# Optimization experiments

Measured on AMD Instinct MI355X. Metric: run time of the kernel, lower is better.

## Reference

```python
import jax, jax.numpy as jnp
import numpy as np

L, H, N, F, E, FF, OUT, B = 4, 8, 1024, 128, 128, 512, 64, 32


def setup_inputs() -> dict:
    key = jax.random.key(0)
    ks = jax.random.split(key, 16)
    s = 0.02
    return {
        "x": jax.random.normal(ks[0], (B, N, F), jnp.float32),
        "adj": jax.random.randint(ks[1], (N, N), 0, 2, jnp.int32),
        "Ws": jax.random.normal(ks[2], (L, H, E, F), jnp.float32) * s,
        "bs": jnp.zeros((L, H, E), jnp.float32),
        "As": jax.random.normal(ks[3], (L, H, 2 * E, N), jnp.float32) * s,
        "W1": jax.random.normal(ks[4], (L, FF, F), jnp.float32) * s,
        "b1": jnp.zeros((L, FF), jnp.float32),
        "W2": jax.random.normal(ks[5], (L, F, FF), jnp.float32) * s,
        "b2": jnp.zeros((L, F), jnp.float32),
        "g1": jnp.ones((L, F), jnp.float32),
        "be1": jnp.zeros((L, F), jnp.float32),
        "g2": jnp.ones((L, F), jnp.float32),
        "be2": jnp.zeros((L, F), jnp.float32),
        "Wo": jax.random.normal(ks[6], (OUT, N * F), jnp.float32) * s,
        "bo": jnp.zeros((OUT,), jnp.float32),
    }


def _ln(x, g, b, eps=1e-5):
    m = jnp.mean(x, axis=-1, keepdims=True)
    v = jnp.mean((x - m) ** 2, axis=-1, keepdims=True)
    return (x - m) / jnp.sqrt(v + eps) * g + b


def reference(x, adj, Ws, bs, As, W1, b1, W2, b2, g1, be1, g2, be2, Wo, bo):
    # mask[j, i] = 1 if j is a neighbor of i (adj_matrix[:, i] > 0 in torch source)
    mask = (adj > 0).astype(x.dtype)
    E_ = Ws.shape[2]
    for l in range(Ws.shape[0]):
        # per-head projection: h [B, H, N, E]
        h = jnp.einsum('bnf,hef->bhne', x, Ws[l]) + bs[l][None, :, None, :]
        # score[b,h,i] = h_i . a[:E, i] + (sum_{j in N(i)} h_j) . a[E:, i]
        s1 = jnp.einsum('bhne,hen->bhn', h, As[l][:, :E_, :])
        hn = jnp.einsum('jn,bhje->bhne', mask, h)  # neighbor sums
        s2 = jnp.einsum('bhne,hen->bhn', hn, As[l][:, E_:, :])
        score = s1 + s2  # [B, H, N]
        # attention row i is the constant score[b,h,i] broadcast over columns,
        # so attention @ h == score[...,None] * h.sum(over nodes)
        hsum = h.sum(axis=2)  # [B, H, E]
        hp = score[..., None] * hsum[:, :, None, :]  # [B, H, N, E]
        att = jax.nn.leaky_relu(hp, 0.01).sum(axis=1)  # sum over heads -> [B, N, F]
        x = _ln(x + att, g1[l], be1[l])
        ff = jax.nn.relu(x @ W1[l].T + b1[l]) @ W2[l].T + b2[l]
        x = _ln(x + ff, g2[l], be2[l])
    flat = x.reshape(x.shape[0], -1)  # [B, N*F]
    return jax.nn.relu(flat) @ Wo.T + bo
```

## Files before the change

### kernel.cpp

```cpp
#include <hip/hip_runtime.h>

#define L_ 4
#define H_ 8
#define Nn 1024
#define F_ 128
#define E_ 128
#define FF_ 512
#define OUT_ 64
#define B_ 32
#define KTOT (Nn * F_)

typedef unsigned short u16;
typedef __bf16 bf16_t;
typedef __attribute__((ext_vector_type(8))) __bf16 bf16x8;
typedef __attribute__((ext_vector_type(4))) float f32x4;

__device__ __forceinline__ u16 f2b(float v) {
    bf16_t h = (bf16_t)v;
    return __builtin_bit_cast(u16, h);
}

typedef const __attribute__((address_space(1))) void* gvp;
typedef __attribute__((address_space(3))) void* lvp;
__device__ __forceinline__ void gll16(const void* g, void* l) {
    __builtin_amdgcn_global_load_lds((gvp)g, (lvp)l, 16, 0, 0);
}

template <int R>
__device__ __forceinline__ void stage(const u16* __restrict__ g, int ldg,
                                      u16* lds, int w, int l) {
    const int r8 = l >> 3, jq = l & 7;
#pragma unroll
    for (int i = 0; i < R / 32; ++i) {
        const int row0 = w * (R / 4) + i * 8;
        const int row = row0 + r8;
        gll16(g + (long)row * ldg + ((jq ^ (row & 7)) << 3), lds + row0 * 64);
    }
}

template <int BM, int BN, bool DUAL, int EPI, int BSH, bool GSWAP, bool DBUF>
__global__ __launch_bounds__(256) void k_mfma(
    const u16* __restrict__ A, int lda, long sAz,
    const u16* __restrict__ Bhp, const u16* __restrict__ Blp, int ldb, long sBz,
    const float* __restrict__ bias,
    float* __restrict__ Cf, u16* __restrict__ Cb, int ldc, long sCz, int K)
{
    constexpr int WN = (BN == 64) ? 1 : ((BM == 64) ? 4 : 2);
    constexpr int WM = 4 / WN;
    constexpr int SM = BM / WM, SN = BN / WN;
    constexpr int MF = SM / 16, NF = SN / 16;
    constexpr int BUFE = BM * 64 + (DUAL ? 2 : 1) * BN * 64;
    __shared__ __align__(16) u16 lds[BUFE * (DBUF ? 2 : 1)];
    const int t = threadIdx.x;
    const int w = t >> 6, l = t & 63, lr = l & 15, lg = l >> 4;
    const int wm0 = (w / WN) * SM, wn0 = (w % WN) * SN;
    const int bidm = GSWAP ? blockIdx.z : blockIdx.x;
    const int bidz = GSWAP ? blockIdx.x : blockIdx.z;
    const int m0 = bidm * BM, n0 = blockIdx.y * BN;
    A += BSH ? ((long)(bidz >> 1) * sAz + (long)(bidz & 1) * 128)
             : (long)bidz * sAz;
    Bhp += (long)(bidz >> BSH) * sBz;
    if (DUAL) Blp += (long)bidz * sBz;

    f32x4 acc[MF][NF] = {};

    auto stageAll = [&](u16* base, int k0) {
        stage<BM>(A + (long)m0 * lda + k0, lda, base, w, l);
        stage<BN>(Bhp + (long)n0 * ldb + k0, ldb, base + BM * 64, w, l);
        if (DUAL) stage<BN>(Blp + (long)n0 * ldb + k0, ldb, base + BM * 64 + BN * 64, w, l);
    };
    auto compute = [&](const u16* base) {
        const u16* Al = base;
        const u16* Bh = base + BM * 64;
        const u16* Bl = Bh + BN * 64;
#pragma unroll
        for (int ks = 0; ks < 2; ++ks) {
            bf16x8 af[MF], bh[NF], bl[NF];
            const int kq = ks * 4 + lg;
#pragma unroll
            for (int mf = 0; mf < MF; ++mf) {
                int row = wm0 + mf * 16 + lr;
                af[mf] = *reinterpret_cast<const bf16x8*>(&Al[row * 64 + ((kq ^ (row & 7)) << 3)]);
            }
#pragma unroll
            for (int nf = 0; nf < NF; ++nf) {
                int row = wn0 + nf * 16 + lr;
                int off = row * 64 + ((kq ^ (row & 7)) << 3);
                bh[nf] = *reinterpret_cast<const bf16x8*>(&Bh[off]);
                if (DUAL) bl[nf] = *reinterpret_cast<const bf16x8*>(&Bl[off]);
            }
#pragma unroll
            for (int mf = 0; mf < MF; ++mf)
#pragma unroll
                for (int nf = 0; nf < NF; ++nf) {
                    acc[mf][nf] = __builtin_amdgcn_mfma_f32_16x16x32_bf16(af[mf], bh[nf], acc[mf][nf], 0, 0, 0);
                    if (DUAL)
                        acc[mf][nf] = __builtin_amdgcn_mfma_f32_16x16x32_bf16(af[mf], bl[nf], acc[mf][nf], 0, 0, 0);
                }
        }
    };

    if (DBUF) {
        stageAll(lds, 0);
        __syncthreads();
        int cur = 0;
        for (int k0 = 0; k0 < K; k0 += 64) {
            if (k0 + 64 < K) stageAll(lds + (cur ^ 1) * BUFE, k0 + 64);
            compute(lds + cur * BUFE);
            __syncthreads();
            cur ^= 1;
        }
    } else {
        for (int k0 = 0; k0 < K; k0 += 64) {
            __syncthreads();
            stageAll(lds, k0);
            __syncthreads();
            compute(lds);
        }
    }

    float bv[NF];
    if (EPI) {
#pragma unroll
        for (int nf = 0; nf < NF; ++nf) bv[nf] = bias[n0 + wn0 + nf * 16 + lr];
    }
    if (EPI == 1) Cb += (long)bidz * sCz;
    else          Cf += (long)bidz * sCz;
#pragma unroll
    for (int mf = 0; mf < MF; ++mf)
#pragma unroll
        for (int nf = 0; nf < NF; ++nf)
#pragma unroll
            for (int r = 0; r < 4; ++r) {
                long row = m0 + wm0 + mf * 16 + lg * 4 + r;
                int col = n0 + wn0 + nf * 16 + lr;
                float v = acc[mf][nf][r];
                if (EPI) v += bv[nf];
                if (EPI == 1) Cb[row * ldc + col] = f2b(fmaxf(v, 0.f));
                else          Cf[row * ldc + col] = v;
            }
}

template <bool LAST>
__global__ __launch_bounds__(256) void k_ff_ln2(
    const u16* __restrict__ xb,
    const u16* __restrict__ W1b,
    const float* __restrict__ b1,
    const u16* __restrict__ W2b,
    const float* __restrict__ b2,
    float* __restrict__ xc,
    const float* __restrict__ g, const float* __restrict__ be,
    u16* __restrict__ xh, u16* __restrict__ xl,
    float* __restrict__ xsp,
    u16* __restrict__ xrb)
{
    __shared__ __align__(16) u16 lds[18432];
    const int t = threadIdx.x;
    const int w = t >> 6, l = t & 63, lr = l & 15, lg = l >> 4;
    const int wn0 = w * 32;
    const int m0 = blockIdx.x * 64;
    u16* A0 = lds;
    u16* P0 = lds + 8192;

    stage<64>(xb + (long)m0 * F_,      F_, A0, w, l);
    stage<64>(xb + (long)m0 * F_ + 64, F_, A0 + 4096, w, l);
    __syncthreads();

    f32x4 acc2[4][2] = {};
    for (int c = 0; c < 4; ++c) {
        f32x4 acc1[4][2] = {};
#pragma unroll
        for (int s = 0; s < 4; ++s) {
            const int kh = s >> 1, kq = (s & 1) * 4 + lg;
            bf16x8 af[4], bfr[2];
#pragma unroll
            for (int mf = 0; mf < 4; ++mf) {
                int row = mf * 16 + lr;
                af[mf] = *reinterpret_cast<const bf16x8*>(
                    &A0[kh * 4096 + row * 64 + ((kq ^ (row & 7)) << 3)]);
            }
#pragma unroll
            for (int nf = 0; nf < 2; ++nf) {
                int row = c * 128 + wn0 + nf * 16 + lr;
                bfr[nf] = *reinterpret_cast<const bf16x8*>(
                    &W1b[(long)row * F_ + s * 32 + lg * 8]);
            }
#pragma unroll
            for (int mf = 0; mf < 4; ++mf)
#pragma unroll
                for (int nf = 0; nf < 2; ++nf)
                    acc1[mf][nf] = __builtin_amdgcn_mfma_f32_16x16x32_bf16(af[mf], bfr[nf], acc1[mf][nf], 0, 0, 0);
        }
        __syncthreads();
        float b1v[2] = { b1[c * 128 + wn0 + lr], b1[c * 128 + wn0 + 16 + lr] };
#pragma unroll
        for (int mf = 0; mf < 4; ++mf)
#pragma unroll
            for (int nf = 0; nf < 2; ++nf)
#pragma unroll
                for (int r = 0; r < 4; ++r) {
                    int row = mf * 16 + lg * 4 + r;
                    int cc = wn0 + nf * 16 + lr;
                    int c6 = cc & 63;
                    float v = fmaxf(acc1[mf][nf][r] + b1v[nf], 0.f);
                    P0[(cc >> 6) * 4096 + row * 64 + ((((c6 >> 3) ^ (row & 7))) << 3) + (c6 & 7)] = f2b(v);
                }
        __syncthreads();
#pragma unroll
        for (int s = 0; s < 4; ++s) {
            const int kh = s >> 1, kq = (s & 1) * 4 + lg;
            bf16x8 af[4], bfr[2];
#pragma unroll
            for (int mf = 0; mf < 4; ++mf) {
                int row = mf * 16 + lr;
                af[mf] = *reinterpret_cast<const bf16x8*>(
                    &P0[kh * 4096 + row * 64 + ((kq ^ (row & 7)) << 3)]);
            }
#pragma unroll
            for (int nf = 0; nf < 2; ++nf) {
                int row = wn0 + nf * 16 + lr;
                bfr[nf] = *reinterpret_cast<const bf16x8*>(
                    &W2b[(long)row * FF_ + c * 128 + s * 32 + lg * 8]);
            }
#pragma unroll
            for (int mf = 0; mf < 4; ++mf)
#pragma unroll
                for (int nf = 0; nf < 2; ++nf)
                    acc2[mf][nf] = __builtin_amdgcn_mfma_f32_16x16x32_bf16(af[mf], bfr[nf], acc2[mf][nf], 0, 0, 0);
        }
    }
    __syncthreads();
    float (*buf)[132] = (float(*)[132])lds;
    float (*ps)[128]  = (float(*)[128])((char*)lds + 34816);
    float bv[2] = { b2[wn0 + lr], b2[wn0 + 16 + lr] };
#pragma unroll
    for (int mf = 0; mf < 4; ++mf)
#pragma unroll
        for (int nf = 0; nf < 2; ++nf)
#pragma unroll
            for (int r = 0; r < 4; ++r)
                buf[mf * 16 + lg * 4 + r][wn0 + nf * 16 + lr] = acc2[mf][nf][r] + bv[nf];
    __syncthreads();
    const float gl0 = g[l], gl1 = g[l + 64], bl0 = be[l], bl1 = be[l + 64];
    float s0 = 0.f, s1 = 0.f;
#pragma unroll
    for (int rr = 0; rr < 16; ++rr) {
        const int row = w * 16 + rr;
        const long xb_ = (long)(m0 + row) * F_;
        float v0 = buf[row][l] + xc[xb_ + l];
        float v1 = buf[row][l + 64] + xc[xb_ + l + 64];
        float sum = v0 + v1;
#pragma unroll
        for (int o = 32; o; o >>= 1) sum += __shfl_xor(sum, o);
        const float mean = sum * (1.f / 128.f);
        const float d0 = v0 - mean, d1 = v1 - mean;
        float vs = d0 * d0 + d1 * d1;
#pragma unroll
        for (int o = 32; o; o >>= 1) vs += __shfl_xor(vs, o);
        const float rstd = rsqrtf(vs * (1.f / 128.f) + 1e-5f);
        float o0 = d0 * rstd * gl0 + bl0;
        float o1 = d1 * rstd * gl1 + bl1;
        if (LAST) {
            xrb[xb_ + l] = f2b(fmaxf(o0, 0.f));
            xrb[xb_ + l + 64] = f2b(fmaxf(o1, 0.f));
        } else {
            xc[xb_ + l] = o0;       xc[xb_ + l + 64] = o1;
            buf[row][l] = o0;       buf[row][l + 64] = o1;
            s0 += o0;               s1 += o1;
        }
    }
    if (!LAST) {
        ps[w][l] = s0; ps[w][l + 64] = s1;
        __syncthreads();
        const int b = m0 >> 10, nb0 = m0 & 1023, seg = (m0 >> 6) & 15;
        const int n8 = (t & 7) * 8, fb = t >> 3;
#pragma unroll
        for (int i = 0; i < 4; ++i) {
            const int f = fb + 32 * i;
            union { u16 u[8]; float4 v; } Hv, Lv;
#pragma unroll
            for (int j = 0; j < 8; ++j) {
                float v = buf[n8 + j][f];
                bf16_t h = (bf16_t)v;
                Hv.u[j] = __builtin_bit_cast(u16, h);
                Lv.u[j] = f2b(v - (float)h);
            }
            const long ob = ((long)b * F_ + f) * Nn + nb0 + n8;
            *reinterpret_cast<float4*>(&xh[ob]) = Hv.v;
            *reinterpret_cast<float4*>(&xl[ob]) = Lv.v;
        }
        if (t < 128)
            xsp[((long)b * 16 + seg) * 128 + t] =
                ps[0][t] + ps[1][t] + ps[2][t] + ps[3][t];
    }
}

__global__ __launch_bounds__(256) void k_final_mfma(
    const u16* __restrict__ xrb, const u16* __restrict__ Wob,
    float* __restrict__ part)
{
    __shared__ __align__(16) u16 Al[32 * 512];
    const int c = blockIdx.x;
    const long k0 = (long)c * 512;
    const int t = threadIdx.x, w = t >> 6, l = t & 63, lr = l & 15, lg = l >> 4;
#pragma unroll
    for (int i = 0; i < 8; ++i) {
        int ch = i * 256 + t, row = ch >> 6, jq = ch & 63;
        *reinterpret_cast<float4*>(&Al[row * 512 + ((jq ^ (row & 7)) << 3)]) =
            *reinterpret_cast<const float4*>(&xrb[(long)row * KTOT + k0 + (jq << 3)]);
    }
    __syncthreads();
    f32x4 acc[2] = {};
    const u16* Bp = Wob + (long)(w * 16 + lr) * KTOT + k0 + lg * 8;
#pragma unroll
    for (int ks = 0; ks < 16; ++ks) {
        bf16x8 bfr = *reinterpret_cast<const bf16x8*>(Bp + ks * 32);
        const int j8 = ks * 4 + lg;
#pragma unroll
        for (int mf = 0; mf < 2; ++mf) {
            int row = mf * 16 + lr;
            bf16x8 af = *reinterpret_cast<const bf16x8*>(&Al[row * 512 + ((j8 ^ (row & 7)) << 3)]);
            acc[mf] = __builtin_amdgcn_mfma_f32_16x16x32_bf16(af, bfr, acc[mf], 0, 0, 0);
        }
    }
#pragma unroll
    for (int mf = 0; mf < 2; ++mf)
#pragma unroll
        for (int r = 0; r < 4; ++r) {
            int b = mf * 16 + lg * 4 + r, o = w * 16 + lr;
            part[((long)c * B_ + b) * OUT_ + o] = acc[mf][r];
        }
}

__global__ void k_final_reduce(const float* __restrict__ part,
                               const float* __restrict__ bo, float* __restrict__ out)
{
    int i = blockIdx.x * 256 + threadIdx.x;
    int o = i & 63;
    float s = bo[o];
    for (int c = 0; c < 256; ++c) s += part[(long)c * (B_ * OUT_) + i];
    out[i] = s;
}

__global__ __launch_bounds__(256) void k_maskT(const int* __restrict__ adj,
                                               u16* __restrict__ maskTb,
                                               int* __restrict__ degi)
{
    __shared__ u16 tl[64][65];
    const int j0 = blockIdx.x * 64, n0 = blockIdx.y * 64, t = threadIdx.x;
#pragma unroll
    for (int i = 0; i < 16; ++i) {
        int s = i * 256 + t, jl = s >> 6, nl = s & 63;
        tl[jl][nl] = (adj[(long)(j0 + jl) * Nn + n0 + nl] > 0) ? 0x3F80 : 0;
    }
    __syncthreads();
    if (t < 64) {
        int c = 0;
#pragma unroll
        for (int jl = 0; jl < 64; ++jl) c += (tl[jl][t] != 0);
        atomicAdd(&degi[n0 + t], c);
    }
#pragma unroll
    for (int i = 0; i < 16; ++i) {
        int s = i * 256 + t, nl = s >> 6, jl = s & 63;
        maskTb[(long)(n0 + nl) * Nn + j0 + jl] = tl[jl][nl];
    }
}

__global__ __launch_bounds__(256) void k_tpb(const float* __restrict__ in,
                                             u16* __restrict__ out, int R, int C)
{
    __shared__ float tl[64][65];
    const int c0 = blockIdx.x * 64, r0 = blockIdx.y * 64, t = threadIdx.x;
    in  += (long)blockIdx.z * R * C;
    out += (long)blockIdx.z * R * C;
#pragma unroll
    for (int i = 0; i < 16; ++i) {
        int s = i * 256 + t, rl = s >> 6, cl = s & 63;
        tl[rl][cl] = in[(long)(r0 + rl) * C + c0 + cl];
    }
    __syncthreads();
#pragma unroll
    for (int i = 0; i < 16; ++i) {
        int s = i * 256 + t, cl = s >> 6, rl = s & 63;
        out[(long)(c0 + cl) * R + r0 + rl] = f2b(tl[rl][cl]);
    }
}

__global__ void k_cvtW(const float* __restrict__ W1, const float* __restrict__ W2,
                       u16* __restrict__ W1b, u16* __restrict__ W2b)
{
    int i = blockIdx.x * 256 + threadIdx.x;
    W1b[i] = f2b(W1[i]);
    W2b[i] = f2b(W2[i]);
}

__global__ void k_cvtWo(const float* __restrict__ Wo, u16* __restrict__ Wob)
{
    long i = ((long)blockIdx.x * 256 + threadIdx.x) * 8;
    float4 a = *reinterpret_cast<const float4*>(&Wo[i]);
    float4 b = *reinterpret_cast<const float4*>(&Wo[i + 4]);
    union { u16 u[8]; float4 v; } r;
    r.u[0] = f2b(a.x); r.u[1] = f2b(a.y); r.u[2] = f2b(a.z); r.u[3] = f2b(a.w);
    r.u[4] = f2b(b.x); r.u[5] = f2b(b.y); r.u[6] = f2b(b.z); r.u[7] = f2b(b.w);
    *reinterpret_cast<float4*>(&Wob[i]) = r.v;
}

__global__ __launch_bounds__(256) void k_xpose(const float* __restrict__ x,
                                               u16* __restrict__ xh, u16* __restrict__ xl)
{
    __shared__ float tile[64][132];
    const int b = blockIdx.y, n0 = blockIdx.x * 64, t = threadIdx.x;
#pragma unroll
    for (int i = 0; i < 8; ++i) {
        int s = i * 256 + t, nl = s >> 5, f4 = (s & 31) << 2;
        float4 v = *reinterpret_cast<const float4*>(&x[((long)b * Nn + n0 + nl) * F_ + f4]);
        tile[nl][f4] = v.x; tile[nl][f4 + 1] = v.y;
        tile[nl][f4 + 2] = v.z; tile[nl][f4 + 3] = v.w;
    }
    __syncthreads();
    const int f = t >> 1, nb = (t & 1) << 5;
    const long ob = ((long)b * F_ + f) * Nn + n0 + nb;
    union { u16 u[8]; float4 v; } Hv, Lv;
#pragma unroll
    for (int i = 0; i < 32; i += 8) {
#pragma unroll
        for (int j = 0; j < 8; ++j) {
            float v = tile[nb + i + j][f];
            bf16_t h = (bf16_t)v;
            Hv.u[j] = __builtin_bit_cast(u16, h);
            Lv.u[j] = f2b(v - (float)h);
        }
        *reinterpret_cast<float4*>(&xh[ob + i]) = Hv.v;
        *reinterpret_cast<float4*>(&xl[ob + i]) = Lv.v;
    }
}

__global__ __launch_bounds__(256) void k_xs2(const float* __restrict__ x, float* __restrict__ xsp)
{
    __shared__ float sh[2][128];
    const int seg = blockIdx.x, b = blockIdx.y, t = threadIdx.x;
    const int f = t & 127, h2 = t >> 7;
    const float* p = x + ((long)b * Nn + seg * 64 + h2 * 32) * F_ + f;
    float s = 0.f;
    for (int i = 0; i < 32; ++i) s += p[(long)i * F_];
    sh[h2][f] = s;
    __syncthreads();
    if (t < 128) xsp[((long)b * 16 + seg) * 128 + t] = sh[0][t] + sh[1][t];
}

__global__ void k_hsum(const float* __restrict__ xsp, const float* __restrict__ Wl,
                       const float* __restrict__ bsl, float* __restrict__ hsum)
{
    __shared__ float xs[128];
    const int i = blockIdx.x * 256 + threadIdx.x;
    const int b = i >> 10;
    if (threadIdx.x < 128) {
        const float* xp = xsp + (long)b * 16 * 128 + threadIdx.x;
        float v = 0.f;
#pragma unroll
        for (int sg = 0; sg < 16; ++sg) v += xp[sg * 128];
        xs[threadIdx.x] = v;
    }
    __syncthreads();
    const int e = i & 127, h = (i >> 7) & 7;
    const float* w = Wl + ((long)h * E_ + e) * F_;
    float s = 0.f;
    for (int f = 0; f < F_; ++f) s += xs[f] * w[f];
    hsum[i] = s + (float)Nn * bsl[h * E_ + e];
}

__global__ void k_d12(const float* __restrict__ As, const float* __restrict__ bs,
                      float* __restrict__ d12all)
{
    const int lyr = blockIdx.y;
    const float* Asl = As + (long)lyr * H_ * 2 * E_ * Nn;
    const float* bsl = bs + (long)lyr * H_ * E_;
    int i = blockIdx.x * 256 + threadIdx.x;
    int n = i & 1023, h = (i >> 10) & 7, w = i >> 13;
    const float* a = Asl + ((long)h * 2 * E_ + (long)w * E_) * Nn + n;
    const float* bb = bsl + h * E_;
    float s = 0.f;
    for (int e = 0; e < E_; ++e) s += bb[e] * a[(long)e * Nn];
    d12all[(long)lyr * 2 * H_ * Nn + ((long)w * H_ + h) * Nn + n] = s;
}

__global__ __launch_bounds__(256) void k_score_ln1(
    float* __restrict__ x, const float* __restrict__ y,
    const float* __restrict__ Ct, const float* __restrict__ d12,
    const int* __restrict__ degi, const float* __restrict__ hsum,
    const float* __restrict__ g, const float* __restrict__ be,
    u16* __restrict__ xb)
{
    const int n = blockIdx.x, t = threadIdx.x;
    __shared__ float c1[H_][128], c2[H_][128];
    __shared__ float sbs[H_];
#pragma unroll
    for (int i = 0; i < 4; ++i) {
        int s = i * 256 + t, h = s >> 7, f = s & 127;
        c1[h][f] = Ct[((long)(2 * h) * Nn + n) * F_ + f];
        c2[h][f] = Ct[((long)(2 * h + 1) * Nn + n) * F_ + f];
    }
    if (t < H_) sbs[t] = d12[(long)t * Nn + n] + (float)degi[n] * d12[(long)(H_ + t) * Nn + n];
    __syncthreads();
    const int w = t >> 6, l = t & 63;
    const float gl0 = g[l], gl1 = g[l + 64], bl0 = be[l], bl1 = be[l + 64];
    for (int bi = 0; bi < 8; ++bi) {
        const int b = w * 8 + bi;
        const long base = ((long)b * Nn + n) * F_;
        float x0 = x[base + l], x1 = x[base + l + 64];
        float y0 = y[base + l], y1 = y[base + l + 64];
        float a0 = 0.f, a1 = 0.f;
#pragma unroll
        for (int h = 0; h < H_; ++h) {
            float p = x0 * c1[h][l] + x1 * c1[h][l + 64]
                    + y0 * c2[h][l] + y1 * c2[h][l + 64];
#pragma unroll
            for (int o = 32; o; o >>= 1) p += __shfl_xor(p, o);
            float s = p + sbs[h];
            float h0 = hsum[((long)b * H_ + h) * E_ + l];
            float h1 = hsum[((long)b * H_ + h) * E_ + l + 64];
            float p0 = s * h0, p1 = s * h1;
            a0 += (p0 > 0.f ? p0 : 0.01f * p0);
            a1 += (p1 > 0.f ? p1 : 0.01f * p1);
        }
        float v0 = x0 + a0, v1 = x1 + a1;
        float sum = v0 + v1;
#pragma unroll
        for (int o = 32; o; o >>= 1) sum += __shfl_xor(sum, o);
        const float mean = sum * (1.f / 128.f);
        const float d0 = v0 - mean, d1 = v1 - mean;
        float vs = d0 * d0 + d1 * d1;
#pragma unroll
        for (int o = 32; o; o >>= 1) vs += __shfl_xor(vs, o);
        const float rstd = rsqrtf(vs * (1.f / 128.f) + 1e-5f);
        float o0 = d0 * rstd * gl0 + bl0;
        float o1 = d1 * rstd * gl1 + bl1;
        x[base + l] = o0;        x[base + l + 64] = o1;
        xb[base + l] = f2b(o0);  xb[base + l + 64] = f2b(o1);
    }
}

extern "C" void kernel_launch(void* const* d_in, const int* in_sizes, int n_in,
                              void* d_out, int out_size, void* d_ws, size_t ws_size,
                              hipStream_t stream)
{
    const float* x_in = (const float*)d_in[0];
    const int*   adj  = (const int*)d_in[1];
    const float* Ws   = (const float*)d_in[2];
    const float* bs   = (const float*)d_in[3];
    const float* As   = (const float*)d_in[4];
    const float* W1   = (const float*)d_in[5];
    const float* b1   = (const float*)d_in[6];
    const float* W2   = (const float*)d_in[7];
    const float* b2   = (const float*)d_in[8];
    const float* g1   = (const float*)d_in[9];
    const float* be1  = (const float*)d_in[10];
    const float* g2   = (const float*)d_in[11];
    const float* be2  = (const float*)d_in[12];
    const float* Wo   = (const float*)d_in[13];
    const float* bo   = (const float*)d_in[14];
    float* out = (float*)d_out;

    char* wsb = (char*)d_ws;
    u16*   maskTb = (u16*)wsb;
    float* xc     = (float*)(wsb + (2L << 20));
    float* y      = (float*)(wsb + (18L << 20));
    float* CtAll  = (float*)(wsb + (66L << 20));
    u16*   xb     = (u16*)(wsb + (98L << 20));
    u16*   xrb    = (u16*)(wsb + (106L << 20));
    u16*   Wob    = (u16*)(wsb + (114L << 20));
    float* part   = (float*)(wsb + (130L << 20));
    u16*   xTh    = (u16*)(wsb + (132L << 20));
    u16*   xTl    = (u16*)(wsb + (140L << 20));
    u16*   AsTb   = (u16*)(wsb + (148L << 20));
    u16*   WsTb   = (u16*)(wsb + (164L << 20));
    char*  S      = wsb + (166L << 20);
    int*   degi   = (int*)S;
    float* xsp    = (float*)(S + (4L << 10));
    float* hsum   = (float*)(S + (260L << 10));
    float* d12all = (float*)(S + (388L << 10));
    u16*   W1b    = (u16*)(S + (644L << 10));
    u16*   W2b    = (u16*)(S + (1156L << 10));

    hipMemsetAsync(degi, 0, Nn * sizeof(int), stream);
    hipMemcpyAsync(xc, x_in, sizeof(float) * (long)B_ * Nn * F_,
                   hipMemcpyDeviceToDevice, stream);
    k_maskT<<<dim3(16, 16), 256, 0, stream>>>(adj, maskTb, degi);
    k_cvtW<<<(L_ * FF_ * F_) / 256, 256, 0, stream>>>(W1, W2, W1b, W2b);
    k_cvtWo<<<(OUT_ * KTOT) / (256 * 8), 256, 0, stream>>>(Wo, Wob);
    k_tpb<<<dim3(16, 4, L_ * H_), 256, 0, stream>>>(As, AsTb, 2 * E_, Nn);
    k_tpb<<<dim3(2, 2, L_ * H_), 256, 0, stream>>>(Ws, WsTb, E_, F_);
    k_xpose<<<dim3(16, B_), 256, 0, stream>>>(x_in, xTh, xTl);
    k_xs2<<<dim3(16, B_), 256, 0, stream>>>(x_in, xsp);
    k_d12<<<dim3((2 * H_ * Nn) / 256, L_), 256, 0, stream>>>(As, bs, d12all);
    k_mfma<64, 128, false, 0, 1, false, false><<<dim3(16, 1, 64), 256, 0, stream>>>(
        AsTb, 2 * E_, (long)Nn * 2 * E_, WsTb, nullptr, E_, (long)F_ * E_,
        nullptr, CtAll, nullptr, F_, (long)Nn * F_, E_);

    for (int l = 0; l < L_; ++l) {
        const float* Wl  = Ws + (long)l * H_ * E_ * F_;
        const float* bsl = bs + (long)l * H_ * E_;

        k_mfma<128, 64, true, 0, 0, true, true><<<dim3(32, 2, 8), 256, 0, stream>>>(
            maskTb, Nn, 0L, xTh, xTl, Nn, (long)F_ * Nn,
            nullptr, y, nullptr, F_, (long)Nn * F_, Nn);

        k_hsum<<<(B_ * H_ * E_) / 256, 256, 0, stream>>>(xsp, Wl, bsl, hsum);
        k_score_ln1<<<Nn, 256, 0, stream>>>(
            xc, y, CtAll + (long)l * 16 * Nn * F_, d12all + (long)l * 2 * H_ * Nn,
            degi, hsum, g1 + l * F_, be1 + l * F_, xb);
        if (l < L_ - 1)
            k_ff_ln2<false><<<512, 256, 0, stream>>>(
                xb, W1b + (long)l * FF_ * F_, b1 + l * FF_,
                W2b + (long)l * F_ * FF_, b2 + l * F_, xc,
                g2 + l * F_, be2 + l * F_, xTh, xTl, xsp, nullptr);
        else
            k_ff_ln2<true><<<512, 256, 0, stream>>>(
                xb, W1b + (long)l * FF_ * F_, b1 + l * FF_,
                W2b + (long)l * F_ * FF_, b2 + l * F_, xc,
                g2 + l * F_, be2 + l * F_, nullptr, nullptr, nullptr, xrb);
    }

    k_final_mfma<<<256, 256, 0, stream>>>(xrb, Wob, part);
    k_final_reduce<<<(B_ * OUT_) / 256, 256, 0, stream>>>(part, bo, out);
}
```

Baseline: 412.2 us.

## Give each wave its own 16 rows in fused FFN+LN kernel, dropping block barriers

Restructures the fused FFN/LayerNorm kernel so each wave owns 16 rows and computes all 128 output columns, with weights as the MFMA A operand and activations as B (a transposed product). The hidden activation goes through a private per-wave LDS slice, which removes the block-wide __syncthreads between GEMM phases. LayerNorm now runs directly on the accumulator registers with vectorized residual and parameter loads, instead of going through an LDS staging buffer. In exchange, each wave reads four times as many weight fragments from global/L2, and the column-sum reduction becomes a 64-row serial loop over LDS.

```diff
diff --git a/kernel.cpp b/kernel.cpp
--- a/kernel.cpp
+++ b/kernel.cpp
@@ -154,123 +154,114 @@
     float* __restrict__ xsp,
     u16* __restrict__ xrb)
 {
-    __shared__ __align__(16) u16 lds[18432];
+    __shared__ __align__(16) u16 lds[16896];
     const int t = threadIdx.x;
     const int w = t >> 6, l = t & 63, lr = l & 15, lg = l >> 4;
-    const int wn0 = w * 32;
     const int m0 = blockIdx.x * 64;
-    u16* A0 = lds;
-    u16* P0 = lds + 8192;
-
-    stage<64>(xb + (long)m0 * F_,      F_, A0, w, l);
-    stage<64>(xb + (long)m0 * F_ + 64, F_, A0 + 4096, w, l);
-    __syncthreads();
-
-    f32x4 acc2[4][2] = {};
+    const int M0 = m0 + w * 16;
+    u16* xw = lds + w * 2048;
+    u16* pw = lds + 8192 + w * 2176;
+
+    {
+        const int r8 = l >> 3, jq = l & 7;
+#pragma unroll
+        for (int h = 0; h < 2; ++h)
+#pragma unroll
+            for (int i = 0; i < 2; ++i) {
+                const int row = i * 8 + r8;
+                gll16(xb + (long)(M0 + row) * F_ + h * 64 + ((jq ^ (row & 7)) << 3),
+                      xw + h * 1024 + i * 512);
+            }
+    }
+    asm volatile("s_waitcnt vmcnt(0)" ::: "memory");
+
+    f32x4 acc2[8] = {};
     for (int c = 0; c < 4; ++c) {
-        f32x4 acc1[4][2] = {};
+        f32x4 acc1[8] = {};
 #pragma unroll
         for (int s = 0; s < 4; ++s) {
             const int kh = s >> 1, kq = (s & 1) * 4 + lg;
-            bf16x8 af[4], bfr[2];
-#pragma unroll
-            for (int mf = 0; mf < 4; ++mf) {
-                int row = mf * 16 + lr;
-                af[mf] = *reinterpret_cast<const bf16x8*>(
-                    &A0[kh * 4096 + row * 64 + ((kq ^ (row & 7)) << 3)]);
+            bf16x8 xf = *reinterpret_cast<const bf16x8*>(
+                &xw[kh * 1024 + lr * 64 + ((kq ^ (lr & 7)) << 3)]);
+#pragma unroll
+            for (int nf = 0; nf < 8; ++nf) {
+                bf16x8 wf = *reinterpret_cast<const bf16x8*>(
+                    &W1b[(long)(c * 128 + nf * 16 + lr) * F_ + s * 32 + lg * 8]);
+                acc1[nf] = __builtin_amdgcn_mfma_f32_16x16x32_bf16(wf, xf, acc1[nf], 0, 0, 0);
             }
-#pragma unroll
-            for (int nf = 0; nf < 2; ++nf) {
-                int row = c * 128 + wn0 + nf * 16 + lr;
-                bfr[nf] = *reinterpret_cast<const bf16x8*>(
-                    &W1b[(long)row * F_ + s * 32 + lg * 8]);
+        }
+#pragma unroll
+        for (int nf = 0; nf < 8; ++nf) {
+            f32x4 bb = *reinterpret_cast<const f32x4*>(&b1[c * 128 + nf * 16 + lg * 4]);
+            union { u16 u[4]; uint2 q; } pk;
+#pragma unroll
+            for (int r = 0; r < 4; ++r)
+                pk.u[r] = f2b(fmaxf(acc1[nf][r] + bb[r], 0.f));
+            *reinterpret_cast<uint2*>(&pw[lr * 136 + nf * 16 + lg * 4]) = pk.q;
+        }
+#pragma unroll
+        for (int s2 = 0; s2 < 4; ++s2) {
+            bf16x8 pf = *reinterpret_cast<const bf16x8*>(&pw[lr * 136 + s2 * 32 + lg * 8]);
+#pragma unroll
+            for (int nf = 0; nf < 8; ++nf) {
+                bf16x8 wf = *reinterpret_cast<const bf16x8*>(
+                    &W2b[(long)(nf * 16 + lr) * FF_ + c * 128 + s2 * 32 + lg * 8]);
+                acc2[nf] = __builtin_amdgcn_mfma_f32_16x16x32_bf16(wf, pf, acc2[nf], 0, 0, 0);
             }
-#pragma unroll
-            for (int mf = 0; mf < 4; ++mf)
-#pragma unroll
-                for (int nf = 0; nf < 2; ++nf)
-                    acc1[mf][nf] = __builtin_amdgcn_mfma_f32_16x16x32_bf16(af[mf], bfr[nf], acc1[mf][nf], 0, 0, 0);
-        }
+        }
+    }
+
+    const long Mrow = (long)M0 + lr;
+    f32x4 vv[8];
+    float sum = 0.f;
+#pragma unroll
+    for (int nf = 0; nf < 8; ++nf) {
+        f32x4 rsd = *reinterpret_cast<const f32x4*>(&xc[Mrow * F_ + nf * 16 + lg * 4]);
+        f32x4 bb  = *reinterpret_cast<const f32x4*>(&b2[nf * 16 + lg * 4]);
+#pragma unroll
+        for (int r = 0; r < 4; ++r) {
+            vv[nf][r] = acc2[nf][r] + bb[r] + rsd[r];
+            sum += vv[nf][r];
+        }
+    }
+    sum += __shfl_xor(sum, 16);
+    sum += __shfl_xor(sum, 32);
+    const float mean = sum * (1.f / 128.f);
+    float vs = 0.f;
+#pragma unroll
+    for (int nf = 0; nf < 8; ++nf)
+#pragma unroll
+        for (int r = 0; r < 4; ++r) {
+            float d = vv[nf][r] - mean;
+            vs += d * d;
+        }
+    vs += __shfl_xor(vs, 16);
+    vs += __shfl_xor(vs, 32);
+    const float rstd = rsqrtf(vs * (1.f / 128.f) + 1e-5f);
+#pragma unroll
+    for (int nf = 0; nf < 8; ++nf) {
+        f32x4 gg = *reinterpret_cast<const f32x4*>(&g[nf * 16 + lg * 4]);
+        f32x4 bz = *reinterpret_cast<const f32x4*>(&be[nf * 16 + lg * 4]);
+        f32x4 o;
+#pragma unroll
+        for (int r = 0; r < 4; ++r)
+            o[r] = (vv[nf][r] - mean) * rstd * gg[r] + bz[r];
+        if (LAST) {
+            union { u16 u[4]; uint2 q; } pk;
+#pragma unroll
+            for (int r = 0; r < 4; ++r) pk.u[r] = f2b(fmaxf(o[r], 0.f));
+            *reinterpret_cast<uint2*>(&xrb[Mrow * F_ + nf * 16 + lg * 4]) = pk.q;
+        } else {
+            *reinterpret_cast<f32x4*>(&xc[Mrow * F_ + nf * 16 + lg * 4]) = o;
+            vv[nf] = o;
+        }
+    }
+    if (!LAST) {
         __syncthreads();
-        float b1v[2] = { b1[c * 128 + wn0 + lr], b1[c * 128 + wn0 + 16 + lr] };
-#pragma unroll
-        for (int mf = 0; mf < 4; ++mf)
-#pragma unroll
-            for (int nf = 0; nf < 2; ++nf)
-#pragma unroll
-                for (int r = 0; r < 4; ++r) {
-                    int row = mf * 16 + lg * 4 + r;
-                    int cc = wn0 + nf * 16 + lr;
-                    int c6 = cc & 63;
-                    float v = fmaxf(acc1[mf][nf][r] + b1v[nf], 0.f);
-                    P0[(cc >> 6) * 4096 + row * 64 + ((((c6 >> 3) ^ (row & 7))) << 3) + (c6 & 7)] = f2b(v);
-                }
-        __syncthreads();
-#pragma unroll
-        for (int s = 0; s < 4; ++s) {
-            const int kh = s >> 1, kq = (s & 1) * 4 + lg;
-            bf16x8 af[4], bfr[2];
-#pragma unroll
-            for (int mf = 0; mf < 4; ++mf) {
-                int row = mf * 16 + lr;
-                af[mf] = *reinterpret_cast<const bf16x8*>(
-                    &P0[kh * 4096 + row * 64 + ((kq ^ (row & 7)) << 3)]);
-            }
-#pragma unroll
-            for (int nf = 0; nf < 2; ++nf) {
-                int row = wn0 + nf * 16 + lr;
-                bfr[nf] = *reinterpret_cast<const bf16x8*>(
-                    &W2b[(long)row * FF_ + c * 128 + s * 32 + lg * 8]);
-            }
-#pragma unroll
-            for (int mf = 0; mf < 4; ++mf)
-#pragma unroll
-                for (int nf = 0; nf < 2; ++nf)
-                    acc2[mf][nf] = __builtin_amdgcn_mfma_f32_16x16x32_bf16(af[mf], bfr[nf], acc2[mf][nf], 0, 0, 0);
-        }
-    }
-    __syncthreads();
-    float (*buf)[132] = (float(*)[132])lds;
-    float (*ps)[128]  = (float(*)[128])((char*)lds + 34816);
-    float bv[2] = { b2[wn0 + lr], b2[wn0 + 16 + lr] };
-#pragma unroll
-    for (int mf = 0; mf < 4; ++mf)
-#pragma unroll
-        for (int nf = 0; nf < 2; ++nf)
-#pragma unroll
-            for (int r = 0; r < 4; ++r)
-                buf[mf * 16 + lg * 4 + r][wn0 + nf * 16 + lr] = acc2[mf][nf][r] + bv[nf];
-    __syncthreads();
-    const float gl0 = g[l], gl1 = g[l + 64], bl0 = be[l], bl1 = be[l + 64];
-    float s0 = 0.f, s1 = 0.f;
-#pragma unroll
-    for (int rr = 0; rr < 16; ++rr) {
-        const int row = w * 16 + rr;
-        const long xb_ = (long)(m0 + row) * F_;
-        float v0 = buf[row][l] + xc[xb_ + l];
-        float v1 = buf[row][l + 64] + xc[xb_ + l + 64];
-        float sum = v0 + v1;
-#pragma unroll
-        for (int o = 32; o; o >>= 1) sum += __shfl_xor(sum, o);
-        const float mean = sum * (1.f / 128.f);
-        const float d0 = v0 - mean, d1 = v1 - mean;
-        float vs = d0 * d0 + d1 * d1;
-#pragma unroll
-        for (int o = 32; o; o >>= 1) vs += __shfl_xor(vs, o);
-        const float rstd = rsqrtf(vs * (1.f / 128.f) + 1e-5f);
-        float o0 = d0 * rstd * gl0 + bl0;
-        float o1 = d1 * rstd * gl1 + bl1;
-        if (LAST) {
-            xrb[xb_ + l] = f2b(fmaxf(o0, 0.f));
-            xrb[xb_ + l + 64] = f2b(fmaxf(o1, 0.f));
-        } else {
-            xc[xb_ + l] = o0;       xc[xb_ + l + 64] = o1;
-            buf[row][l] = o0;       buf[row][l + 64] = o1;
-            s0 += o0;               s1 += o1;
-        }
-    }
-    if (!LAST) {
-        ps[w][l] = s0; ps[w][l + 64] = s1;
+        float (*buf)[132] = (float(*)[132])lds;
+#pragma unroll
+        for (int nf = 0; nf < 8; ++nf)
+            *reinterpret_cast<f32x4*>(&buf[w * 16 + lr][nf * 16 + lg * 4]) = vv[nf];
         __syncthreads();
         const int b = m0 >> 10, nb0 = m0 & 1023, seg = (m0 >> 6) & 15;
         const int n8 = (t & 7) * 8, fb = t >> 3;
@@ -289,9 +280,12 @@
             *reinterpret_cast<float4*>(&xh[ob]) = Hv.v;
             *reinterpret_cast<float4*>(&xl[ob]) = Lv.v;
         }
-        if (t < 128)
-            xsp[((long)b * 16 + seg) * 128 + t] =
-                ps[0][t] + ps[1][t] + ps[2][t] + ps[3][t];
+        if (t < 128) {
+            float s = 0.f;
+#pragma unroll
+            for (int r = 0; r < 64; ++r) s += buf[r][t];
+            xsp[((long)b * 16 + seg) * 128 + t] = s;
+        }
     }
 }
 
```

Result: slower. 571.1 us (+38.6%).
